# Performance work log

Measured on AMD Instinct MI355X. Metric: run time of the kernel, lower is better.

## Reference

```python
import jax, jax.numpy as jnp
import numpy as np

N_NODES = 50000
N_EDGES = 800000
DIM = 64
HIDDEN = 256


def setup_inputs() -> dict:
    key = jax.random.key(0)
    k_h, k_src, k_dst, k_w1, k_w2 = jax.random.split(key, 5)
    h = jax.random.normal(k_h, (N_NODES, DIM), dtype=jnp.float32)
    src = jax.random.randint(k_src, (N_EDGES,), 0, N_NODES, dtype=jnp.int64)
    dst = jax.random.randint(k_dst, (N_EDGES,), 0, N_NODES, dtype=jnp.int64)
    edge_index = jnp.stack([src, dst], axis=0)
    # Kaiming-ish init scale for the MLP weights
    W1 = jax.random.normal(k_w1, (2 * DIM, HIDDEN), dtype=jnp.float32) * (1.0 / np.sqrt(2 * DIM))
    b1 = jnp.zeros((HIDDEN,), dtype=jnp.float32)
    W2 = jax.random.normal(k_w2, (HIDDEN, DIM), dtype=jnp.float32) * (1.0 / np.sqrt(HIDDEN))
    b2 = jnp.zeros((DIM,), dtype=jnp.float32)
    return {"h": h, "edge_index": edge_index, "W1": W1, "b1": b1, "W2": W2, "b2": b2}


def reference(h, edge_index, W1, b1, W2, b2):
    n = h.shape[0]
    src, dst = edge_index[0], edge_index[1]
    # scatter-sum of neighbor features and degree counts into dst nodes
    agg = jax.ops.segment_sum(h[src], dst, num_segments=n)          # [N, D]
    deg = jax.ops.segment_sum(jnp.ones((src.shape[0],), h.dtype), dst, num_segments=n)  # [N]
    mean = agg / jnp.maximum(deg, 1.0)[:, None]
    # isolated nodes (deg == 0) keep their own features
    agg = jnp.where((deg == 0)[:, None], h, mean)
    x = jnp.concatenate([h, agg], axis=-1)                          # [N, 2D]
    # 2-layer MLP with exact (erf) GELU, matching torch nn.GELU default
    hid = jax.nn.gelu(x @ W1 + b1, approximate=False)               # [N, H]
    return hid @ W2 + b2                                            # [N, D]
```

## Files before the change

### kernel.cpp

```cpp
#include <hip/hip_runtime.h>
#include <cstdint>

#define N_NODES 50000
#define N_EDGES 800000
#define DIM 64
#define HIDDEN 256

#define NCB 196
#define EPA 2048
#define ABLKS ((N_EDGES + EPA - 1) / EPA)
#define MAXBE 5120

typedef __attribute__((ext_vector_type(8))) short bf16x8;
typedef __attribute__((ext_vector_type(4))) float f32x4;

__device__ __forceinline__ unsigned short bf16_rne(float f) {
    union { float f; uint32_t u; } cv; cv.f = f;
    uint32_t u = cv.u;
    u += 0x7FFFu + ((u >> 16) & 1u);
    return (unsigned short)(u >> 16);
}

__device__ __forceinline__ float bf2f(unsigned short us) {
    union { uint32_t u; float f; } cv; cv.u = ((uint32_t)us) << 16;
    return cv.f;
}

__device__ __forceinline__ float gelu_f(float v) {
    float u = v * (0.7978845608028654f + 0.035677408136300125f * v * v);
    float e = __expf(fmaxf(fminf(2.0f * u, 80.0f), -80.0f));
    float th = (e - 1.0f) / (e + 1.0f);
    return 0.5f * v * (1.0f + th);
}

#define PREP_TOTAL (N_NODES * DIM + 128 * 256 + 256 * 64)
__global__ __launch_bounds__(256)
void prep_kernel(const float* __restrict__ h, const float* __restrict__ W1,
                 const float* __restrict__ W2, unsigned short* __restrict__ xb,
                 unsigned short* __restrict__ w1t, unsigned short* __restrict__ w2t,
                 int* __restrict__ bcnt) {
    if (blockIdx.x == 0 && threadIdx.x < NCB) bcnt[threadIdx.x] = 0;
    int i4 = (blockIdx.x * 256 + threadIdx.x) * 4;
    if (i4 < N_NODES * DIM) {
        float4 v = *(const float4*)&h[i4];
        ushort4 o;
        o.x = bf16_rne(v.x); o.y = bf16_rne(v.y);
        o.z = bf16_rne(v.z); o.w = bf16_rne(v.w);
        *(ushort4*)&xb[i4] = o;
    } else if (i4 < N_NODES * DIM + 128 * 256) {
        int j = i4 - N_NODES * DIM;
        float4 v = *(const float4*)&W1[j];
        int k = j >> 8, n = j & 255;
        w1t[(n    ) * 128 + k] = bf16_rne(v.x);
        w1t[(n + 1) * 128 + k] = bf16_rne(v.y);
        w1t[(n + 2) * 128 + k] = bf16_rne(v.z);
        w1t[(n + 3) * 128 + k] = bf16_rne(v.w);
    } else if (i4 < PREP_TOTAL) {
        int j = i4 - N_NODES * DIM - 128 * 256;
        float4 v = *(const float4*)&W2[j];
        int jr = j >> 6, d = j & 63;
        w2t[(d    ) * 256 + jr] = bf16_rne(v.x);
        w2t[(d + 1) * 256 + jr] = bf16_rne(v.y);
        w2t[(d + 2) * 256 + jr] = bf16_rne(v.z);
        w2t[(d + 3) * 256 + jr] = bf16_rne(v.w);
    }
}

__global__ __launch_bounds__(256)
void partA_kernel(const int* __restrict__ src, const int* __restrict__ dst,
                  int* __restrict__ bcnt, unsigned int* __restrict__ gbuf) {
    __shared__ unsigned int pairs[EPA];
    __shared__ int cnt[NCB], offs[NCB], wc[NCB], gbase[NCB];

    const int t = threadIdx.x;
    for (int i = t; i < NCB; i += 256) cnt[i] = 0;
    __syncthreads();

    const int base = blockIdx.x * EPA;
    const int ne = (N_EDGES - base < EPA) ? (N_EDGES - base) : EPA;

    #pragma unroll
    for (int i = 0; i < EPA / 256; ++i) {
        int e = t + i * 256;
        if (e < ne) atomicAdd(&cnt[((unsigned)dst[base + e]) >> 8], 1);
    }
    __syncthreads();

    if (t < 64) {
        const int b4 = t * 4;
        int c0 = (b4     < NCB) ? cnt[b4]     : 0;
        int c1 = (b4 + 1 < NCB) ? cnt[b4 + 1] : 0;
        int c2 = (b4 + 2 < NCB) ? cnt[b4 + 2] : 0;
        int c3 = (b4 + 3 < NCB) ? cnt[b4 + 3] : 0;
        const int s = c0 + c1 + c2 + c3;
        int inc = s;
        #pragma unroll
        for (int off = 1; off < 64; off <<= 1) {
            int u = __shfl_up(inc, off, 64);
            if (t >= off) inc += u;
        }
        int ex = inc - s;
        if (b4     < NCB) { offs[b4]     = ex;                wc[b4]     = ex; }
        if (b4 + 1 < NCB) { offs[b4 + 1] = ex + c0;           wc[b4 + 1] = ex + c0; }
        if (b4 + 2 < NCB) { offs[b4 + 2] = ex + c0 + c1;      wc[b4 + 2] = ex + c0 + c1; }
        if (b4 + 3 < NCB) { offs[b4 + 3] = ex + c0 + c1 + c2; wc[b4 + 3] = ex + c0 + c1 + c2; }
    }
    __syncthreads();

    #pragma unroll
    for (int i = 0; i < EPA / 256; ++i) {
        int e = t + i * 256;
        if (e < ne) {
            unsigned int d_ = (unsigned)dst[base + e];
            unsigned int p = (d_ << 16) | (unsigned)src[base + e];
            int pos = atomicAdd(&wc[d_ >> 8], 1);
            pairs[pos] = p;
        }
    }
    __syncthreads();

    if (t < NCB) {
        int c = cnt[t];
        gbase[t] = c ? (t * MAXBE + atomicAdd(&bcnt[t], c)) : 0;
    }
    __syncthreads();

    for (int p = t; p < ne; p += 256) {
        unsigned int pr = pairs[p];
        int b = (int)(pr >> 24);
        int idx = gbase[b] + (p - offs[b]);
        if (idx < (b + 1) * MAXBE) gbuf[idx] = pr;
    }
}

__global__ __launch_bounds__(1024)
void partB_kernel(const unsigned int* __restrict__ gbuf, const int* __restrict__ bcnt,
                  unsigned short* __restrict__ csr16, int2* __restrict__ rng) {
    __shared__ unsigned int ep[MAXBE];
    __shared__ unsigned int so[MAXBE];
    __shared__ int cnt[256], offs[256], wc[256];

    const int t = threadIdx.x;
    const int b = blockIdx.x;
    if (t < 256) cnt[t] = 0;
    __syncthreads();

    const int s0 = b * MAXBE;
    int ne = bcnt[b];
    if (ne > MAXBE) ne = MAXBE;

    for (int i = t; i < ne; i += 1024) {
        unsigned int p = gbuf[s0 + i];
        ep[i] = p;
        atomicAdd(&cnt[(p >> 16) & 255], 1);
    }
    __syncthreads();

    if (t < 64) {
        const int b4 = t * 4;
        int c0 = cnt[b4], c1 = cnt[b4 + 1], c2 = cnt[b4 + 2], c3 = cnt[b4 + 3];
        const int s = c0 + c1 + c2 + c3;
        int inc = s;
        #pragma unroll
        for (int off = 1; off < 64; off <<= 1) {
            int u = __shfl_up(inc, off, 64);
            if (t >= off) inc += u;
        }
        int ex = inc - s;
        offs[b4] = ex;                    wc[b4] = ex;
        offs[b4 + 1] = ex + c0;           wc[b4 + 1] = ex + c0;
        offs[b4 + 2] = ex + c0 + c1;      wc[b4 + 2] = ex + c0 + c1;
        offs[b4 + 3] = ex + c0 + c1 + c2; wc[b4 + 3] = ex + c0 + c1 + c2;
    }
    __syncthreads();

    for (int i = t; i < ne; i += 1024) {
        unsigned int p = ep[i];
        int pos = atomicAdd(&wc[(p >> 16) & 255], 1);
        so[pos] = p;
    }
    __syncthreads();

    for (int i = t; i < ne; i += 1024)
        csr16[s0 + i] = (unsigned short)(so[i] & 0xFFFFu);

    if (t < 256) {
        int node = b * 256 + t;
        if (node < N_NODES) {
            int st = s0 + offs[t];
            rng[node] = make_int2(st, st + cnt[t]);
        }
    }
}

__global__ __launch_bounds__(256, 4)
void gmlp_kernel(const unsigned short* __restrict__ xb,
                 const int2* __restrict__ rng,
                 const unsigned short* __restrict__ csr16,
                 const unsigned short* __restrict__ w1t,
                 const unsigned short* __restrict__ w2t,
                 const float* __restrict__ b1v,
                 const float* __restrict__ b2v,
                 float* __restrict__ out) {
    __shared__ unsigned short xs[32][136];
    __shared__ unsigned short hid[32][264];

    const int tid = threadIdx.x;
    const int w   = tid >> 6;
    const int l   = tid & 63;
    const int l15 = l & 15;
    const int kg  = l >> 4;
    const int node0 = blockIdx.x * 32;

    for (int ni = 0; ni < 8; ++ni) {
        const int n = w * 8 + ni;
        const int node = node0 + n;
        float hv = 0.0f;
        int st = 0, en = 0;
        if (node < N_NODES) {
            hv = bf2f(xb[(size_t)node * 64 + l]);
            int2 rg = rng[node];
            st = rg.x; en = rg.y;
        }
        float acc = 0.0f;
        int i = st;
        for (; i + 7 < en; i += 8) {
            int s0 = csr16[i],     s1 = csr16[i + 1], s2 = csr16[i + 2], s3 = csr16[i + 3];
            int s4 = csr16[i + 4], s5 = csr16[i + 5], s6 = csr16[i + 6], s7 = csr16[i + 7];
            float v0 = bf2f(xb[(size_t)s0 * 64 + l]);
            float v1 = bf2f(xb[(size_t)s1 * 64 + l]);
            float v2 = bf2f(xb[(size_t)s2 * 64 + l]);
            float v3 = bf2f(xb[(size_t)s3 * 64 + l]);
            float v4 = bf2f(xb[(size_t)s4 * 64 + l]);
            float v5 = bf2f(xb[(size_t)s5 * 64 + l]);
            float v6 = bf2f(xb[(size_t)s6 * 64 + l]);
            float v7 = bf2f(xb[(size_t)s7 * 64 + l]);
            acc += ((v0 + v1) + (v2 + v3)) + ((v4 + v5) + (v6 + v7));
        }
        for (; i + 3 < en; i += 4) {
            int s0 = csr16[i], s1 = csr16[i + 1], s2 = csr16[i + 2], s3 = csr16[i + 3];
            float v0 = bf2f(xb[(size_t)s0 * 64 + l]);
            float v1 = bf2f(xb[(size_t)s1 * 64 + l]);
            float v2 = bf2f(xb[(size_t)s2 * 64 + l]);
            float v3 = bf2f(xb[(size_t)s3 * 64 + l]);
            acc += (v0 + v1) + (v2 + v3);
        }
        for (; i < en; ++i) acc += bf2f(xb[(size_t)csr16[i] * 64 + l]);
        const int degc = en - st;
        float mv = (degc > 0) ? (acc / (float)degc) : hv;
        xs[n][l]      = bf16_rne(hv);
        xs[n][64 + l] = bf16_rne(mv);
    }
    __syncthreads();

    f32x4 acc[2][4];
    #pragma unroll
    for (int a = 0; a < 2; ++a)
        #pragma unroll
        for (int b = 0; b < 4; ++b) acc[a][b] = f32x4{0.f, 0.f, 0.f, 0.f};

    #pragma unroll
    for (int s = 0; s < 4; ++s) {
        const int kofs = s * 32 + kg * 8;
        bf16x8 a[2], b[4];
        #pragma unroll
        for (int nt = 0; nt < 2; ++nt)
            a[nt] = *(const bf16x8*)&xs[nt * 16 + l15][kofs];
        #pragma unroll
        for (int jt = 0; jt < 4; ++jt)
            b[jt] = *(const bf16x8*)(w1t + ((w * 4 + jt) * 16 + l15) * 128 + kofs);
        #pragma unroll
        for (int nt = 0; nt < 2; ++nt)
            #pragma unroll
            for (int jt = 0; jt < 4; ++jt)
                acc[nt][jt] = __builtin_amdgcn_mfma_f32_16x16x32_bf16(
                    a[nt], b[jt], acc[nt][jt], 0, 0, 0);
    }

    #pragma unroll
    for (int jt = 0; jt < 4; ++jt) {
        const int jcol = (w * 4 + jt) * 16 + l15;
        float bias = b1v[jcol];
        #pragma unroll
        for (int nt = 0; nt < 2; ++nt) {
            #pragma unroll
            for (int r = 0; r < 4; ++r) {
                float v = acc[nt][jt][r] + bias;
                hid[nt * 16 + kg * 4 + r][jcol] = bf16_rne(gelu_f(v));
            }
        }
    }
    __syncthreads();

    f32x4 acc2[2];
    #pragma unroll
    for (int a = 0; a < 2; ++a) acc2[a] = f32x4{0.f, 0.f, 0.f, 0.f};

    #pragma unroll
    for (int s = 0; s < 8; ++s) {
        const int kofs = s * 32 + kg * 8;
        bf16x8 bb = *(const bf16x8*)(w2t + (w * 16 + l15) * 256 + kofs);
        #pragma unroll
        for (int nt = 0; nt < 2; ++nt) {
            bf16x8 aa = *(const bf16x8*)&hid[nt * 16 + l15][kofs];
            acc2[nt] = __builtin_amdgcn_mfma_f32_16x16x32_bf16(aa, bb, acc2[nt], 0, 0, 0);
        }
    }

    float bias2 = b2v[w * 16 + l15];
    #pragma unroll
    for (int nt = 0; nt < 2; ++nt) {
        #pragma unroll
        for (int r = 0; r < 4; ++r) {
            int node = node0 + nt * 16 + kg * 4 + r;
            if (node < N_NODES)
                out[(size_t)node * DIM + w * 16 + l15] = acc2[nt][r] + bias2;
        }
    }
}

extern "C" void kernel_launch(void* const* d_in, const int* in_sizes, int n_in,
                              void* d_out, int out_size, void* d_ws, size_t ws_size,
                              hipStream_t stream) {
    const float* h  = (const float*)d_in[0];
    const int* eidx = (const int*)d_in[1];
    const float* W1 = (const float*)d_in[2];
    const float* b1 = (const float*)d_in[3];
    const float* W2 = (const float*)d_in[4];
    const float* b2 = (const float*)d_in[5];
    float* out = (float*)d_out;

    const int* src = eidx;
    const int* dst = eidx + N_EDGES;

    unsigned short* xb    = (unsigned short*)d_ws;
    unsigned short* w1t   = xb + (size_t)N_NODES * 64;
    unsigned short* w2t   = w1t + 128 * 256;
    unsigned int*   gbuf  = (unsigned int*)(w2t + 256 * 64);
    unsigned short* csr16 = (unsigned short*)(gbuf + NCB * MAXBE);
    int*  bcnt = (int*)(csr16 + NCB * MAXBE);
    int2* rng  = (int2*)(bcnt + NCB);

    prep_kernel<<<(PREP_TOTAL / 4 + 255) / 256, 256, 0, stream>>>(h, W1, W2, xb, w1t, w2t, bcnt);
    partA_kernel<<<ABLKS, 256, 0, stream>>>(src, dst, bcnt, gbuf);
    partB_kernel<<<NCB, 1024, 0, stream>>>(gbuf, bcnt, csr16, rng);
    {
        int grid = (N_NODES + 31) / 32;
        gmlp_kernel<<<grid, 256, 0, stream>>>(xb, rng, csr16, w1t, w2t, b1, b2, out);
    }
}
```

Measured before the change: 103.3 us.

## Split neighbor gather into separate kernel writing concat buffer for MFMA MLP

Unfuses the mean-aggregation gather from the MLP kernel into its own kernel, one wave per node. Each half-wave handles alternate edges and loads two bf16 features per lane as a 32-bit word, then the halves combine with a shuffle. The result is written into the second half of a widened [N,128] bf16 buffer. The MLP kernel now reads its A operand straight from global memory and raises occupancy, at the cost of an extra launch and a global round trip for the aggregated features.

```diff
diff --git a/kernel.cpp b/kernel.cpp
--- a/kernel.cpp
+++ b/kernel.cpp
@@ -46,7 +46,8 @@
         ushort4 o;
         o.x = bf16_rne(v.x); o.y = bf16_rne(v.y);
         o.z = bf16_rne(v.z); o.w = bf16_rne(v.w);
-        *(ushort4*)&xb[i4] = o;
+        int node = i4 >> 6, d = i4 & 63;
+        *(ushort4*)&xb[(size_t)node * 128 + d] = o;
     } else if (i4 < N_NODES * DIM + 128 * 256) {
         int j = i4 - N_NODES * DIM;
         float4 v = *(const float4*)&W1[j];
@@ -193,16 +194,62 @@
     }
 }
 
-__global__ __launch_bounds__(256, 4)
-void gmlp_kernel(const unsigned short* __restrict__ xb,
-                 const int2* __restrict__ rng,
-                 const unsigned short* __restrict__ csr16,
-                 const unsigned short* __restrict__ w1t,
-                 const unsigned short* __restrict__ w2t,
-                 const float* __restrict__ b1v,
-                 const float* __restrict__ b2v,
-                 float* __restrict__ out) {
-    __shared__ unsigned short xs[32][136];
+__global__ __launch_bounds__(256)
+void gather_kernel(const int2* __restrict__ rng,
+                   const unsigned short* __restrict__ csr16,
+                   unsigned short* __restrict__ xb) {
+    const unsigned int* xbu = (const unsigned int*)xb;
+    int node = blockIdx.x * 4 + (threadIdx.x >> 6);
+    if (node >= N_NODES) return;
+    const int l = threadIdx.x & 63;
+    const int p = l & 31;
+    const int half = l >> 5;
+    int2 rg = rng[node];
+    const int st = rg.x, en = rg.y;
+    const int degc = en - st;
+    float a0 = 0.0f, a1 = 0.0f;
+    int i = st + half;
+    for (; i + 6 < en; i += 8) {
+        int s0 = csr16[i];
+        int s1 = csr16[i + 2];
+        int s2 = csr16[i + 4];
+        int s3 = csr16[i + 6];
+        unsigned int u0 = xbu[(size_t)s0 * 64 + p];
+        unsigned int u1 = xbu[(size_t)s1 * 64 + p];
+        unsigned int u2 = xbu[(size_t)s2 * 64 + p];
+        unsigned int u3 = xbu[(size_t)s3 * 64 + p];
+        a0 += (bf2f((unsigned short)u0) + bf2f((unsigned short)u1))
+            + (bf2f((unsigned short)u2) + bf2f((unsigned short)u3));
+        a1 += (bf2f((unsigned short)(u0 >> 16)) + bf2f((unsigned short)(u1 >> 16)))
+            + (bf2f((unsigned short)(u2 >> 16)) + bf2f((unsigned short)(u3 >> 16)));
+    }
+    for (; i < en; i += 2) {
+        int s = csr16[i];
+        unsigned int u = xbu[(size_t)s * 64 + p];
+        a0 += bf2f((unsigned short)u);
+        a1 += bf2f((unsigned short)(u >> 16));
+    }
+    a0 += __shfl_xor(a0, 32, 64);
+    a1 += __shfl_xor(a1, 32, 64);
+    if (half == 0) {
+        unsigned int res;
+        if (degc > 0) {
+            float inv = 1.0f / (float)degc;
+            res = ((unsigned int)bf16_rne(a1 * inv) << 16) | bf16_rne(a0 * inv);
+        } else {
+            res = xbu[(size_t)node * 64 + p];
+        }
+        ((unsigned int*)xb)[(size_t)node * 64 + 32 + p] = res;
+    }
+}
+
+__global__ __launch_bounds__(256, 6)
+void mlp_mfma_kernel(const unsigned short* __restrict__ xb,
+                     const unsigned short* __restrict__ w1t,
+                     const unsigned short* __restrict__ w2t,
+                     const float* __restrict__ b1v,
+                     const float* __restrict__ b2v,
+                     float* __restrict__ out) {
     __shared__ unsigned short hid[32][264];
 
     const int tid = threadIdx.x;
@@ -212,46 +259,12 @@
     const int kg  = l >> 4;
     const int node0 = blockIdx.x * 32;
 
-    for (int ni = 0; ni < 8; ++ni) {
-        const int n = w * 8 + ni;
-        const int node = node0 + n;
-        float hv = 0.0f;
-        int st = 0, en = 0;
-        if (node < N_NODES) {
-            hv = bf2f(xb[(size_t)node * 64 + l]);
-            int2 rg = rng[node];
-            st = rg.x; en = rg.y;
-        }
-        float acc = 0.0f;
-        int i = st;
-        for (; i + 7 < en; i += 8) {
-            int s0 = csr16[i],     s1 = csr16[i + 1], s2 = csr16[i + 2], s3 = csr16[i + 3];
-            int s4 = csr16[i + 4], s5 = csr16[i + 5], s6 = csr16[i + 6], s7 = csr16[i + 7];
-            float v0 = bf2f(xb[(size_t)s0 * 64 + l]);
-            float v1 = bf2f(xb[(size_t)s1 * 64 + l]);
-            float v2 = bf2f(xb[(size_t)s2 * 64 + l]);
-            float v3 = bf2f(xb[(size_t)s3 * 64 + l]);
-            float v4 = bf2f(xb[(size_t)s4 * 64 + l]);
-            float v5 = bf2f(xb[(size_t)s5 * 64 + l]);
-            float v6 = bf2f(xb[(size_t)s6 * 64 + l]);
-            float v7 = bf2f(xb[(size_t)s7 * 64 + l]);
-            acc += ((v0 + v1) + (v2 + v3)) + ((v4 + v5) + (v6 + v7));
-        }
-        for (; i + 3 < en; i += 4) {
-            int s0 = csr16[i], s1 = csr16[i + 1], s2 = csr16[i + 2], s3 = csr16[i + 3];
-            float v0 = bf2f(xb[(size_t)s0 * 64 + l]);
-            float v1 = bf2f(xb[(size_t)s1 * 64 + l]);
-            float v2 = bf2f(xb[(size_t)s2 * 64 + l]);
-            float v3 = bf2f(xb[(size_t)s3 * 64 + l]);
-            acc += (v0 + v1) + (v2 + v3);
-        }
-        for (; i < en; ++i) acc += bf2f(xb[(size_t)csr16[i] * 64 + l]);
-        const int degc = en - st;
-        float mv = (degc > 0) ? (acc / (float)degc) : hv;
-        xs[n][l]      = bf16_rne(hv);
-        xs[n][64 + l] = bf16_rne(mv);
-    }
-    __syncthreads();
+    int arow[2];
+    #pragma unroll
+    for (int nt = 0; nt < 2; ++nt) {
+        int r = node0 + nt * 16 + l15;
+        arow[nt] = (r < N_NODES) ? r : (N_NODES - 1);
+    }
 
     f32x4 acc[2][4];
     #pragma unroll
@@ -265,7 +278,7 @@
         bf16x8 a[2], b[4];
         #pragma unroll
         for (int nt = 0; nt < 2; ++nt)
-            a[nt] = *(const bf16x8*)&xs[nt * 16 + l15][kofs];
+            a[nt] = *(const bf16x8*)(xb + (size_t)arow[nt] * 128 + kofs);
         #pragma unroll
         for (int jt = 0; jt < 4; ++jt)
             b[jt] = *(const bf16x8*)(w1t + ((w * 4 + jt) * 16 + l15) * 128 + kofs);
@@ -334,7 +347,7 @@
     const int* dst = eidx + N_EDGES;
 
     unsigned short* xb    = (unsigned short*)d_ws;
-    unsigned short* w1t   = xb + (size_t)N_NODES * 64;
+    unsigned short* w1t   = xb + (size_t)N_NODES * 128;
     unsigned short* w2t   = w1t + 128 * 256;
     unsigned int*   gbuf  = (unsigned int*)(w2t + 256 * 64);
     unsigned short* csr16 = (unsigned short*)(gbuf + NCB * MAXBE);
@@ -345,7 +358,11 @@
     partA_kernel<<<ABLKS, 256, 0, stream>>>(src, dst, bcnt, gbuf);
     partB_kernel<<<NCB, 1024, 0, stream>>>(gbuf, bcnt, csr16, rng);
     {
+        int grid = (N_NODES + 3) / 4;
+        gather_kernel<<<grid, 256, 0, stream>>>(rng, csr16, xb);
+    }
+    {
         int grid = (N_NODES + 31) / 32;
-        gmlp_kernel<<<grid, 256, 0, stream>>>(xb, rng, csr16, w1t, w2t, b1, b2, out);
-    }
-}
+        mlp_mfma_kernel<<<grid, 256, 0, stream>>>(xb, w1t, w2t, b1, b2, out);
+    }
+}
```

Measured after the change: 89.36 us. 13.5% less time.
